# Kernel tuning notes

Hardware: AMD Instinct MI355X
Metric: run time of the kernel (lower is better)

The kernel has to match this reference:

```python
import jax, jax.numpy as jnp
import numpy as np

N = 128            # cache entries selected per ray (init arg n)
M = 3 * N          # cache rows
B = 65536          # rays in batch
NUM_SAMPLES = 256  # total samples per ray; inner sampler supplies NUM_SAMPLES - N


def _unit(k, shape):
    v = jax.random.normal(k, shape, dtype=jnp.float32)
    return v / jnp.linalg.norm(v, axis=-1, keepdims=True)


def setup_inputs() -> dict:
    key = jax.random.key(0)
    k0, k1, k2, k3, k4, k5 = jax.random.split(key, 6)
    cache_dirs = _unit(k0, (M, 3))
    cache_mip = jax.random.uniform(k1, (M, 1), dtype=jnp.float32)
    cache_bright = jax.random.uniform(k2, (M, 1), dtype=jnp.float32)
    cache = jnp.concatenate([cache_dirs, cache_mip, cache_bright], axis=1)  # (M,5)
    refdirs = _unit(k3, (B, 3))
    normal = _unit(k4, (B, 3))
    samp_rays = _unit(k5, (B, NUM_SAMPLES - N, 3))
    samp_mipval = jax.random.uniform(jax.random.fold_in(k5, 1), (B, NUM_SAMPLES - N), dtype=jnp.float32)
    return {"cache": cache, "refdirs": refdirs, "normal": normal,
            "samp_rays": samp_rays, "samp_mipval": samp_mipval}


def reference(cache, refdirs, normal, samp_rays, samp_mipval):
    # BrightnessSampler.sample with cache_init=True (n = N cache rays appended).
    cache_dirs = cache[:, :3]      # (M,3)
    cache_mip = cache[:, 3]        # (M,)
    # hemisphere test and directional similarity against every cached ray
    hemi = jnp.einsum('bd,md->bm', normal, cache_dirs)    # (B,M)
    sim = jnp.einsum('bd,md->bm', refdirs, cache_dirs)    # (B,M)
    score = jnp.where(hemi > 0, -sim, jnp.float32(0.0))   # (B,M)
    # torch: inds = argsort(score, dim=1) < n ; boolean-mask gather in original
    # position order. Replicate: keep original positions j where order[b,j] < N.
    order = jnp.argsort(score, axis=1)                    # (B,M)
    mask = order < N
    pos = jnp.where(mask, jnp.arange(M)[None, :], M)
    sel_pos = jnp.sort(pos, axis=1)[:, :N]                # (B,N) ascending original positions
    sel_rays = cache_dirs[sel_pos]                        # (B,N,3)
    sel_mipval = cache_mip[sel_pos]                       # (B,N)
    rays = jnp.concatenate([samp_rays, sel_rays], axis=1)       # (B,NUM_SAMPLES,3)
    mipval = jnp.concatenate([samp_mipval, sel_mipval], axis=1)  # (B,NUM_SAMPLES)
    return rays, mipval
```

## Files before the change

### kernel.cpp

```cpp
#include <hip/hip_runtime.h>

#define NCACHE 384

__device__ __forceinline__ unsigned int sortable_bits(float f) {
    unsigned int u = __float_as_uint(f);
    return (u & 0x80000000u) ? ~u : (u | 0x80000000u);
}

__global__ __launch_bounds__(256) void fused_kernel(
    const float*  __restrict__ cache,
    const float*  __restrict__ refdirs,
    const float*  __restrict__ normal,
    const float4* __restrict__ samp_rays4,
    const float4* __restrict__ samp_mip4,
    float* __restrict__ out, int B)
{
#pragma clang fp contract(off)
    __shared__ float sdx[NCACHE], sdy[NCACHE], sdz[NCACHE], smip[NCACHE];
    __shared__ unsigned int bitmap[4][12];

    const int tid  = threadIdx.x;
    const int wave = tid >> 6;
    const int lane = tid & 63;
    const int b    = blockIdx.x * 4 + wave;

    const int b0 = blockIdx.x * 4;
    const int i0 = tid, i1 = tid + 256;
    const int bb0 = b0 + (i0 >> 7), off0 = i0 & 127;
    const int bb1 = b0 + (i1 >> 7), off1 = i1 & 127;
    const float4 c0 = (off0 < 96) ? samp_rays4[(size_t)bb0 * 96 + off0]
                                  : samp_mip4[(size_t)bb0 * 32 + (off0 - 96)];
    const float4 c1 = (off1 < 96) ? samp_rays4[(size_t)bb1 * 96 + off1]
                                  : samp_mip4[(size_t)bb1 * 32 + (off1 - 96)];

    for (int m = tid; m < NCACHE; m += 256) {
        sdx[m]  = cache[m * 5 + 0];
        sdy[m]  = cache[m * 5 + 1];
        sdz[m]  = cache[m * 5 + 2];
        smip[m] = cache[m * 5 + 3];
    }
    if (tid < 48) (&bitmap[0][0])[tid] = 0u;

    const float nx = normal[b * 3 + 0], ny = normal[b * 3 + 1], nz = normal[b * 3 + 2];
    const float rx = refdirs[b * 3 + 0], ry = refdirs[b * 3 + 1], rz = refdirs[b * 3 + 2];

    __syncthreads();

    unsigned int svhi[6];
#pragma unroll
    for (int c = 0; c < 6; ++c) {
        const int m = c * 64 + lane;
        float dx = sdx[m], dy = sdy[m], dz = sdz[m];
        float hemi = __builtin_fmaf(nz, dz, __builtin_fmaf(ny, dy, nx * dx));
        float sim  = __builtin_fmaf(rz, dz, __builtin_fmaf(ry, dy, rx * dx));
        float val  = (hemi > 0.0f) ? -sim : 0.0f;
        val = val + 0.0f;
        svhi[c] = sortable_bits(val);
    }
    const unsigned long long key0 =
        ((unsigned long long)svhi[0] << 32) | (unsigned int)lane;
    const unsigned long long key1 =
        ((unsigned long long)svhi[1] << 32) | (unsigned int)(lane + 64);

    unsigned int r0 = 0, r1 = 0;
#pragma unroll
    for (int c2 = 0; c2 < 6; ++c2) {
#pragma unroll
        for (int l = 0; l < 64; ++l) {
            const unsigned int jh =
                (unsigned int)__builtin_amdgcn_readlane((int)svhi[c2], l);
            const unsigned long long kj =
                ((unsigned long long)jh << 32) | (unsigned int)(c2 * 64 + l);
            asm("v_cmp_lt_u64 vcc, %[kj], %[k0]\n\t"
                "v_addc_co_u32 %[r0], vcc, 0, %[r0], vcc\n\t"
                "v_cmp_lt_u64 vcc, %[kj], %[k1]\n\t"
                "v_addc_co_u32 %[r1], vcc, 0, %[r1], vcc"
                : [r0] "+v"(r0), [r1] "+v"(r1)
                : [kj] "s"(kj), [k0] "v"(key0), [k1] "v"(key1)
                : "vcc");
        }
    }

    atomicOr(&bitmap[wave][r0 >> 5], 1u << (r0 & 31));
    atomicOr(&bitmap[wave][r1 >> 5], 1u << (r1 & 31));

    float* out_rays = out;
    float* out_mip  = out + (size_t)B * 768;

    {
        const int wi = (int)r0 >> 5;
        int s = __popc(bitmap[wave][wi] & ((1u << (r0 & 31)) - 1u));
        for (int w = 0; w < wi; ++w) s += __popc(bitmap[wave][w]);
        const size_t rb = (size_t)b * 768 + 384 + (size_t)s * 3;
        out_rays[rb + 0] = sdx[r0];
        out_rays[rb + 1] = sdy[r0];
        out_rays[rb + 2] = sdz[r0];
        out_mip[(size_t)b * 256 + 128 + s] = smip[r0];
    }
    {
        const int wi = (int)r1 >> 5;
        int s = __popc(bitmap[wave][wi] & ((1u << (r1 & 31)) - 1u));
        for (int w = 0; w < wi; ++w) s += __popc(bitmap[wave][w]);
        const size_t rb = (size_t)b * 768 + 384 + (size_t)s * 3;
        out_rays[rb + 0] = sdx[r1];
        out_rays[rb + 1] = sdy[r1];
        out_rays[rb + 2] = sdz[r1];
        out_mip[(size_t)b * 256 + 128 + s] = smip[r1];
    }

    float4* out4     = (float4*)out;
    float4* out_mip4 = (float4*)(out + (size_t)B * 768);
    if (off0 < 96) out4[(size_t)bb0 * 192 + off0] = c0;
    else           out_mip4[(size_t)bb0 * 64 + (off0 - 96)] = c0;
    if (off1 < 96) out4[(size_t)bb1 * 192 + off1] = c1;
    else           out_mip4[(size_t)bb1 * 64 + (off1 - 96)] = c1;
}

extern "C" void kernel_launch(void* const* d_in, const int* in_sizes, int n_in,
                              void* d_out, int out_size, void* d_ws, size_t ws_size,
                              hipStream_t stream) {
    const float* cache       = (const float*)d_in[0];
    const float* refdirs     = (const float*)d_in[1];
    const float* normal      = (const float*)d_in[2];
    const float* samp_rays   = (const float*)d_in[3];
    const float* samp_mipval = (const float*)d_in[4];
    float* out = (float*)d_out;

    const int B = in_sizes[1] / 3;

    fused_kernel<<<B / 4, 256, 0, stream>>>(cache, refdirs, normal,
                                            (const float4*)samp_rays,
                                            (const float4*)samp_mipval,
                                            out, B);
}
```

Measured before the change: 247.2 us.

## Rank via LDS broadcast with 32-bit compares plus separate tie-break pass

Each wave now writes its 384 sortable score keys to shared memory and reads them back as uint4 broadcasts. Ranks are computed with 32-bit compares instead of 64-bit compares against readlane'd scalar keys. Ties on equal keys are resolved in a second pass over the first 128 entries using index comparisons, which keeps the stable ordering. This removes the readlane/SGPR pressure and the cost of 64-bit compares, at the price of extra LDS traffic and an additional equality pass.

```diff
diff --git a/kernel.cpp b/kernel.cpp
--- a/kernel.cpp
+++ b/kernel.cpp
@@ -17,6 +17,7 @@
 {
 #pragma clang fp contract(off)
     __shared__ float sdx[NCACHE], sdy[NCACHE], sdz[NCACHE], smip[NCACHE];
+    __shared__ __align__(16) unsigned int vals[4][NCACHE];
     __shared__ unsigned int bitmap[4][12];
 
     const int tid  = threadIdx.x;
@@ -46,7 +47,7 @@
 
     __syncthreads();
 
-    unsigned int svhi[6];
+    unsigned int vk0 = 0, vk1 = 0;
 #pragma unroll
     for (int c = 0; c < 6; ++c) {
         const int m = c * 64 + lane;
@@ -55,30 +56,61 @@
         float sim  = __builtin_fmaf(rz, dz, __builtin_fmaf(ry, dy, rx * dx));
         float val  = (hemi > 0.0f) ? -sim : 0.0f;
         val = val + 0.0f;
-        svhi[c] = sortable_bits(val);
+        const unsigned int sv = sortable_bits(val);
+        vals[wave][m] = sv;
+        if (c == 0) vk0 = sv;
+        if (c == 1) vk1 = sv;
     }
-    const unsigned long long key0 =
-        ((unsigned long long)svhi[0] << 32) | (unsigned int)lane;
-    const unsigned long long key1 =
-        ((unsigned long long)svhi[1] << 32) | (unsigned int)(lane + 64);
 
+    const uint4* v4 = (const uint4*)&vals[wave][0];
     unsigned int r0 = 0, r1 = 0;
 #pragma unroll
-    for (int c2 = 0; c2 < 6; ++c2) {
+    for (int jc = 0; jc < NCACHE / 4; ++jc) {
+        const uint4 q = v4[jc];
+        asm("v_cmp_lt_u32 vcc, %[va], %[k0]\n\t"
+            "v_addc_co_u32 %[r0], vcc, 0, %[r0], vcc\n\t"
+            "v_cmp_lt_u32 vcc, %[va], %[k1]\n\t"
+            "v_addc_co_u32 %[r1], vcc, 0, %[r1], vcc\n\t"
+            "v_cmp_lt_u32 vcc, %[vb], %[k0]\n\t"
+            "v_addc_co_u32 %[r0], vcc, 0, %[r0], vcc\n\t"
+            "v_cmp_lt_u32 vcc, %[vb], %[k1]\n\t"
+            "v_addc_co_u32 %[r1], vcc, 0, %[r1], vcc\n\t"
+            "v_cmp_lt_u32 vcc, %[vc], %[k0]\n\t"
+            "v_addc_co_u32 %[r0], vcc, 0, %[r0], vcc\n\t"
+            "v_cmp_lt_u32 vcc, %[vc], %[k1]\n\t"
+            "v_addc_co_u32 %[r1], vcc, 0, %[r1], vcc\n\t"
+            "v_cmp_lt_u32 vcc, %[vd], %[k0]\n\t"
+            "v_addc_co_u32 %[r0], vcc, 0, %[r0], vcc\n\t"
+            "v_cmp_lt_u32 vcc, %[vd], %[k1]\n\t"
+            "v_addc_co_u32 %[r1], vcc, 0, %[r1], vcc"
+            : [r0] "+v"(r0), [r1] "+v"(r1)
+            : [va] "v"(q.x), [vb] "v"(q.y), [vc] "v"(q.z), [vd] "v"(q.w),
+              [k0] "v"(vk0), [k1] "v"(vk1)
+            : "vcc");
+    }
+
+    const unsigned int ulane = (unsigned int)lane;
 #pragma unroll
-        for (int l = 0; l < 64; ++l) {
-            const unsigned int jh =
-                (unsigned int)__builtin_amdgcn_readlane((int)svhi[c2], l);
-            const unsigned long long kj =
-                ((unsigned long long)jh << 32) | (unsigned int)(c2 * 64 + l);
-            asm("v_cmp_lt_u64 vcc, %[kj], %[k0]\n\t"
-                "v_addc_co_u32 %[r0], vcc, 0, %[r0], vcc\n\t"
-                "v_cmp_lt_u64 vcc, %[kj], %[k1]\n\t"
-                "v_addc_co_u32 %[r1], vcc, 0, %[r1], vcc"
-                : [r0] "+v"(r0), [r1] "+v"(r1)
-                : [kj] "s"(kj), [k0] "v"(key0), [k1] "v"(key1)
-                : "vcc");
-        }
+    for (int jc = 0; jc < 16; ++jc) {
+        const uint4 q = v4[jc];
+        const unsigned int jb = jc * 4;
+        r0 += (q.x == vk0 && jb + 0 < ulane) ? 1u : 0u;
+        r0 += (q.y == vk0 && jb + 1 < ulane) ? 1u : 0u;
+        r0 += (q.z == vk0 && jb + 2 < ulane) ? 1u : 0u;
+        r0 += (q.w == vk0 && jb + 3 < ulane) ? 1u : 0u;
+        r1 += (q.x == vk1) ? 1u : 0u;
+        r1 += (q.y == vk1) ? 1u : 0u;
+        r1 += (q.z == vk1) ? 1u : 0u;
+        r1 += (q.w == vk1) ? 1u : 0u;
+    }
+#pragma unroll
+    for (int jc = 16; jc < 32; ++jc) {
+        const uint4 q = v4[jc];
+        const unsigned int jb = (jc - 16) * 4;
+        r1 += (q.x == vk1 && jb + 0 < ulane) ? 1u : 0u;
+        r1 += (q.y == vk1 && jb + 1 < ulane) ? 1u : 0u;
+        r1 += (q.z == vk1 && jb + 2 < ulane) ? 1u : 0u;
+        r1 += (q.w == vk1 && jb + 3 < ulane) ? 1u : 0u;
     }
 
     atomicOr(&bitmap[wave][r0 >> 5], 1u << (r0 & 31));
```

Measured after the change: 281.8 us. 1.14x slower.
